# Kernel optimization log

Measured on AMD Instinct MI355X. Metric: run time of the kernel, lower is better.

The kernel has to match this reference:

```python
import jax, jax.numpy as jnp
import numpy as np

BETA_MEM = 0.9
BETA_INH = 0.6
THRESHOLD = 1.0  # snn.Leaky default


def setup_inputs() -> dict:
    key = jax.random.key(0)
    k1, = jax.random.split(key, 1)
    T, B = 1024, 16384
    spike_seq = (jax.random.uniform(k1, (T, B, 2)) < 0.05).astype(jnp.float32)
    w_exc = jnp.array([[0.7, 1.0]], dtype=jnp.float32)  # fc_exc.weight, [1, 2]
    w_inh = jnp.array(-1.0, dtype=jnp.float32)          # scalar inhibitory weight
    return {"spike_seq": spike_seq, "w_exc": w_exc, "w_inh": w_inh}


@jax.custom_vjp
def spike_fn(x):
    # Heaviside spike with ATan surrogate gradient (snntorch default, alpha=2)
    return (x > 0).astype(x.dtype)

def _spike_fwd(x):
    return spike_fn(x), x

def _spike_bwd(x, g):
    return (g / (1.0 + (jnp.pi * x) ** 2),)

spike_fn.defvjp(_spike_fwd, _spike_bwd)


def reference(spike_seq, w_exc, w_inh):
    T, B, _ = spike_seq.shape
    mem0 = jnp.zeros((B, 1), dtype=spike_seq.dtype)
    inh0 = jnp.zeros((B, 1), dtype=spike_seq.dtype)

    def step(carry, x_t):
        mem, inh = carry
        cur_exc = x_t @ w_exc.T                      # [B, 1]
        fm1 = x_t[:, 0:1]                            # [B, 1]
        inh = BETA_INH * inh + fm1
        cur = cur_exc + w_inh * inh
        # snn.Leaky: reset (subtract) computed from previous mem, detached
        reset = jax.lax.stop_gradient((mem - THRESHOLD > 0).astype(mem.dtype))
        mem = BETA_MEM * mem + cur - reset * THRESHOLD
        spk = spike_fn(mem - THRESHOLD)
        return (mem, inh), (spk, mem)

    _, (spk_rec, mem_rec) = jax.lax.scan(step, (mem0, inh0), spike_seq)
    return spk_rec, mem_rec  # each [T, B, 1]
```

## Files before the change

kernel.cpp:

```cpp
#include <hip/hip_runtime.h>

#define T_LEN 1024
#define B_N   16384
#define PH    16
#define NPH   (T_LEN / PH)
#define RIN   4


__shared__ __align__(16) float2 IN_lds[RIN][PH][64];
__shared__ __align__(16) float  SPK_lds[2][PH][64];
__shared__ __align__(16) float  MEM_lds[2][PH][64];

static __device__ __forceinline__ void block_barrier() {
  asm volatile("" ::: "memory");
  __builtin_amdgcn_s_barrier();
  asm volatile("" ::: "memory");
}

__global__ __launch_bounds__(256, 1) void FMFMNeuronInhib_34033320854098_kernel(
    const float* __restrict__ x,
    const float* __restrict__ w_exc,
    const float* __restrict__ w_inh,
    float* __restrict__ out) {
#pragma clang fp contract(off)
  const int lane = threadIdx.x & 63;
  const int wid  = threadIdx.x >> 6;
  const int nb0  = blockIdx.x * 64;

  float* __restrict__ spk_out = out;
  float* __restrict__ mem_out = out + (size_t)T_LEN * B_N;

  if (wid == 1) {
    const int half = lane >> 5;
    const int l32  = lane & 31;
    auto issue_phase = [&](int q) {
#pragma unroll
      for (int j = 0; j < 8; ++j) {
        const int t = q * PH + 2 * j + half;
        const float* src = x + ((size_t)t * B_N + nb0) * 2 + (size_t)l32 * 4;
        __builtin_amdgcn_global_load_lds(
            (const __attribute__((address_space(1))) void*)src,
            (__attribute__((address_space(3))) void*)&IN_lds[q & 3][2 * j][0],
            16, 0, 0);
      }
    };
    issue_phase(0); issue_phase(1); issue_phase(2);
    asm volatile("s_waitcnt vmcnt(16)" ::: "memory");
    block_barrier();
    for (int p = 0; p < NPH; ++p) {
      if (p + 3 < NPH) issue_phase(p + 3);
      if (p <= NPH - 4)      asm volatile("s_waitcnt vmcnt(16)" ::: "memory");
      else if (p == NPH - 3) asm volatile("s_waitcnt vmcnt(8)"  ::: "memory");
      else                   asm volatile("s_waitcnt vmcnt(0)"  ::: "memory");
      block_barrier();
    }
  } else if (wid == 0) {
    const float w0 = w_exc[0];
    const float w1 = w_exc[1];
    const float wi = w_inh[0];
    float mem = 0.0f, inh = 0.0f;
    block_barrier();
    for (int p = 0; p < NPH; ++p) {
      float2 xv[PH];
#pragma unroll
      for (int u = 0; u < PH; ++u) xv[u] = IN_lds[p & 3][u][lane];
#pragma unroll
      for (int u = 0; u < PH; ++u) {
        const float x0 = xv[u].x;
        const float x1 = xv[u].y;
        const float cur_exc = x0 * w0 + x1 * w1;
        inh = 0.6f * inh + x0;
        const float cur = cur_exc + wi * inh;
        const float reset = (mem > 1.0f) ? 1.0f : 0.0f;
        mem = 0.9f * mem + cur - reset;
        const float spk = (mem > 1.0f) ? 1.0f : 0.0f;
        SPK_lds[p & 1][u][lane] = spk;
        MEM_lds[p & 1][u][lane] = mem;
      }
      asm volatile("s_waitcnt lgkmcnt(0)" ::: "memory");
      block_barrier();
    }
  } else {
    const float* plane = (wid == 2) ? &SPK_lds[0][0][0] : &MEM_lds[0][0][0];
    float* gout        = (wid == 2) ? spk_out : mem_out;
    const int r  = lane >> 4;
    const int n0 = (lane & 15) * 4;
    auto drain = [&](int p) {
      const int tb   = p * PH;
      const int slot = p & 1;
#pragma unroll
      for (int j = 0; j < 4; ++j) {
        const int row = 4 * j + r;
        const float4 v =
            *(const float4*)(plane + ((size_t)slot * PH + row) * 64 + n0);
        *(float4*)&gout[(size_t)(tb + row) * B_N + nb0 + n0] = v;
      }
      asm volatile("s_waitcnt lgkmcnt(0)" ::: "memory");
    };
    block_barrier();
    for (int p = 0; p < NPH; ++p) {
      if (p >= 1) drain(p - 1);
      block_barrier();
    }
    drain(NPH - 1);
  }
}

extern "C" void kernel_launch(void* const* d_in, const int* in_sizes, int n_in,
                              void* d_out, int out_size, void* d_ws, size_t ws_size,
                              hipStream_t stream) {
  const float* x     = (const float*)d_in[0];
  const float* w_exc = (const float*)d_in[1];
  const float* w_inh = (const float*)d_in[2];
  float* out = (float*)d_out;

  dim3 grid(B_N / 64);
  dim3 block(256);
  hipLaunchKernelGGL(FMFMNeuronInhib_34033320854098_kernel, grid, block, 0, stream,
                     x, w_exc, w_inh, out);
}
```

Before: 229.5 us.

## Widen blocks to 256 neurons and store outputs directly from compute waves

Each block now covers 256 neurons using four compute waves plus one loader wave, instead of 64 neurons with one compute wave. The LDS staging and dedicated drain waves for the spike and membrane outputs are removed, so compute waves write results straight to global memory with coalesced 4-byte stores. The phase shrinks to 8 steps with a 3-slot input ring and prefetch depth 2. This cuts the grid to 64 blocks, which may leave many CUs idle, and makes output stores compete with the serial recurrence in the same waves.

```diff
diff --git a/kernel.cpp b/kernel.cpp
--- a/kernel.cpp
+++ b/kernel.cpp
@@ -2,14 +2,12 @@
 
 #define T_LEN 1024
 #define B_N   16384
-#define PH    16
+#define NB    256
+#define PH    8
 #define NPH   (T_LEN / PH)
-#define RIN   4
+#define RIN   3
 
-
-__shared__ __align__(16) float2 IN_lds[RIN][PH][64];
-__shared__ __align__(16) float  SPK_lds[2][PH][64];
-__shared__ __align__(16) float  MEM_lds[2][PH][64];
+__shared__ __align__(16) float2 IN_lds[RIN][PH][NB];
 
 static __device__ __forceinline__ void block_barrier() {
   asm volatile("" ::: "memory");
@@ -17,7 +15,7 @@
   asm volatile("" ::: "memory");
 }
 
-__global__ __launch_bounds__(256, 1) void FMFMNeuronInhib_34033320854098_kernel(
+__global__ __launch_bounds__(320, 1) void FMFMNeuronInhib_34033320854098_kernel(
     const float* __restrict__ x,
     const float* __restrict__ w_exc,
     const float* __restrict__ w_inh,
@@ -25,47 +23,56 @@
 #pragma clang fp contract(off)
   const int lane = threadIdx.x & 63;
   const int wid  = threadIdx.x >> 6;
-  const int nb0  = blockIdx.x * 64;
+  const int nb0  = blockIdx.x * NB;
 
   float* __restrict__ spk_out = out;
   float* __restrict__ mem_out = out + (size_t)T_LEN * B_N;
 
-  if (wid == 1) {
-    const int half = lane >> 5;
-    const int l32  = lane & 31;
+  if (wid == 4) {
     auto issue_phase = [&](int q) {
+      const int slot = q % RIN;
 #pragma unroll
-      for (int j = 0; j < 8; ++j) {
-        const int t = q * PH + 2 * j + half;
-        const float* src = x + ((size_t)t * B_N + nb0) * 2 + (size_t)l32 * 4;
-        __builtin_amdgcn_global_load_lds(
-            (const __attribute__((address_space(1))) void*)src,
-            (__attribute__((address_space(3))) void*)&IN_lds[q & 3][2 * j][0],
-            16, 0, 0);
+      for (int u = 0; u < PH; ++u) {
+        const int t = q * PH + u;
+#pragma unroll
+        for (int h = 0; h < 2; ++h) {
+          const float* src =
+              x + ((size_t)t * B_N + nb0) * 2 + h * 256 + lane * 4;
+          __builtin_amdgcn_global_load_lds(
+              (const __attribute__((address_space(1))) void*)src,
+              (__attribute__((address_space(3))) void*)&IN_lds[slot][u][h * 128],
+              16, 0, 0);
+        }
       }
     };
-    issue_phase(0); issue_phase(1); issue_phase(2);
+    issue_phase(0);
+    issue_phase(1);
     asm volatile("s_waitcnt vmcnt(16)" ::: "memory");
     block_barrier();
     for (int p = 0; p < NPH; ++p) {
-      if (p + 3 < NPH) issue_phase(p + 3);
-      if (p <= NPH - 4)      asm volatile("s_waitcnt vmcnt(16)" ::: "memory");
-      else if (p == NPH - 3) asm volatile("s_waitcnt vmcnt(8)"  ::: "memory");
-      else                   asm volatile("s_waitcnt vmcnt(0)"  ::: "memory");
+      if (p + 2 < NPH) {
+        issue_phase(p + 2);
+        asm volatile("s_waitcnt vmcnt(16)" ::: "memory");
+      } else {
+        asm volatile("s_waitcnt vmcnt(0)" ::: "memory");
+      }
       block_barrier();
     }
-  } else if (wid == 0) {
+  } else {
     const float w0 = w_exc[0];
     const float w1 = w_exc[1];
     const float wi = w_inh[0];
+    const int nmy = wid * 64 + lane;
     float mem = 0.0f, inh = 0.0f;
     block_barrier();
     for (int p = 0; p < NPH; ++p) {
+      const int slot = p % RIN;
       float2 xv[PH];
 #pragma unroll
-      for (int u = 0; u < PH; ++u) xv[u] = IN_lds[p & 3][u][lane];
+      for (int u = 0; u < PH; ++u) xv[u] = IN_lds[slot][u][nmy];
 #pragma unroll
       for (int u = 0; u < PH; ++u) {
+        const int t = p * PH + u;
         const float x0 = xv[u].x;
         const float x1 = xv[u].y;
         const float cur_exc = x0 * w0 + x1 * w1;
@@ -74,35 +81,13 @@
         const float reset = (mem > 1.0f) ? 1.0f : 0.0f;
         mem = 0.9f * mem + cur - reset;
         const float spk = (mem > 1.0f) ? 1.0f : 0.0f;
-        SPK_lds[p & 1][u][lane] = spk;
-        MEM_lds[p & 1][u][lane] = mem;
+        const size_t idx = (size_t)t * B_N + nb0 + nmy;
+        spk_out[idx] = spk;
+        mem_out[idx] = mem;
       }
       asm volatile("s_waitcnt lgkmcnt(0)" ::: "memory");
       block_barrier();
     }
-  } else {
-    const float* plane = (wid == 2) ? &SPK_lds[0][0][0] : &MEM_lds[0][0][0];
-    float* gout        = (wid == 2) ? spk_out : mem_out;
-    const int r  = lane >> 4;
-    const int n0 = (lane & 15) * 4;
-    auto drain = [&](int p) {
-      const int tb   = p * PH;
-      const int slot = p & 1;
-#pragma unroll
-      for (int j = 0; j < 4; ++j) {
-        const int row = 4 * j + r;
-        const float4 v =
-            *(const float4*)(plane + ((size_t)slot * PH + row) * 64 + n0);
-        *(float4*)&gout[(size_t)(tb + row) * B_N + nb0 + n0] = v;
-      }
-      asm volatile("s_waitcnt lgkmcnt(0)" ::: "memory");
-    };
-    block_barrier();
-    for (int p = 0; p < NPH; ++p) {
-      if (p >= 1) drain(p - 1);
-      block_barrier();
-    }
-    drain(NPH - 1);
   }
 }
 
@@ -114,8 +99,8 @@
   const float* w_inh = (const float*)d_in[2];
   float* out = (float*)d_out;
 
-  dim3 grid(B_N / 64);
-  dim3 block(256);
+  dim3 grid(B_N / NB);
+  dim3 block(320);
   hipLaunchKernelGGL(FMFMNeuronInhib_34033320854098_kernel, grid, block, 0, stream,
                      x, w_exc, w_inh, out);
 }
```

After: 274.1 us. +19.4%, slower.
